# Kernel tuning notes

Measured on AMD Instinct MI355X. Metric: run time of the kernel, lower is better.

## Reference

```python
import jax, jax.numpy as jnp
import numpy as np

USER_NUM = 50000
ITEM_NUM = 50000
N = USER_NUM + ITEM_NUM
VT_DIM = 512
CAT_NUM = 1000
CAT_DIM = 32
HIDDEN = 128
OUT = 64
E = 2_000_000
BAG = 5


def setup_inputs() -> dict:
    key = jax.random.key(0)
    ks = jax.random.split(key, 12)
    inp = {
        "vt_feature": jax.random.normal(ks[0], (ITEM_NUM, VT_DIM), jnp.float32),
        "cat_indices": jax.random.randint(ks[1], (ITEM_NUM * BAG,), 0, CAT_NUM),
        "cat_offsets": jnp.arange(ITEM_NUM) * BAG,
        "edge_index": jax.random.randint(ks[2], (2, E), 0, N),
        # learned parameters
        "cat_table": jax.random.normal(ks[3], (CAT_NUM, CAT_DIM), jnp.float32) * 0.1,
        "fuse_w": jax.random.normal(ks[4], (HIDDEN, VT_DIM + CAT_DIM), jnp.float32) * (1.0 / np.sqrt(VT_DIM + CAT_DIM)),
        "user": jax.random.normal(ks[5], (USER_NUM, HIDDEN), jnp.float32) * 0.1,
        "w1_l": jax.random.normal(ks[6], (HIDDEN, HIDDEN), jnp.float32) * (1.0 / np.sqrt(HIDDEN)),
        "b1": jnp.zeros((HIDDEN,), jnp.float32),
        "w1_r": jax.random.normal(ks[7], (HIDDEN, HIDDEN), jnp.float32) * (1.0 / np.sqrt(HIDDEN)),
        "w2_l": jax.random.normal(ks[8], (OUT, HIDDEN), jnp.float32) * (1.0 / np.sqrt(HIDDEN)),
        "b2": jnp.zeros((OUT,), jnp.float32),
        "w2_r": jax.random.normal(ks[9], (OUT, HIDDEN), jnp.float32) * (1.0 / np.sqrt(HIDDEN)),
    }
    return inp


def _embedding_bag_mean(table, indices, offsets, num_bags):
    # EmbeddingBag(mode='mean') with offsets: segment-mean of table lookups.
    pos = jnp.arange(indices.shape[0])
    seg = jnp.searchsorted(offsets, pos, side="right") - 1  # bag id per index
    sums = jax.ops.segment_sum(table[indices], seg, num_segments=num_bags)
    cnt = jax.ops.segment_sum(jnp.ones_like(pos, jnp.float32), seg, num_segments=num_bags)
    return sums / jnp.maximum(cnt, 1.0)[:, None]


def _sage_conv(x, edge_index, w_l, b_l, w_r):
    # PyG SAGEConv (aggr='mean'): lin_l(mean_{j->i} x_j) + lin_r(x_i)
    src, dst = edge_index[0], edge_index[1]
    agg = jax.ops.segment_sum(x[src], dst, num_segments=N)
    deg = jax.ops.segment_sum(jnp.ones((src.shape[0],), x.dtype), dst, num_segments=N)
    agg = agg / jnp.maximum(deg, 1.0)[:, None]
    return agg @ w_l.T + b_l + x @ w_r.T


def reference(vt_feature, cat_indices, cat_offsets, edge_index, cat_table,
              fuse_w, user, w1_l, b1, w1_r, w2_l, b2, w2_r):
    cat_emb = _embedding_bag_mean(cat_table, cat_indices, cat_offsets, ITEM_NUM)
    item_feat = jnp.concatenate([vt_feature, cat_emb], axis=1) @ fuse_w.T
    x0 = jnp.concatenate([user, item_feat], axis=0)  # [N, hidden]
    x1 = jax.nn.leaky_relu(_sage_conv(x0, edge_index, w1_l, b1, w1_r), negative_slope=0.01)
    # dropout is identity in eval mode
    x2 = _sage_conv(x1, edge_index, w2_l, b2, w2_r)
    return x2
```

## Files before the change

### kernel.cpp

```cpp
#include <hip/hip_runtime.h>

#define USER_N   50000
#define ITEM_N   50000
#define NNODE    100000
#define VT_DIM   512
#define CAT_DIM  32
#define HIDDEN   128
#define OUTD     64
#define PADCAP   64

#define BINC    8192
#define NBKT    98
#define BSHIFT  10
#define SLICES  8

#define AGG_BLOCKS 4096

typedef __attribute__((ext_vector_type(8))) short short8;
typedef __attribute__((ext_vector_type(4))) float f32x4;

__device__ __forceinline__ float bf2f(unsigned short u) {
    return __uint_as_float(((unsigned int)u) << 16);
}
__device__ __forceinline__ unsigned short f2bf(float f) {
    unsigned int u = __float_as_uint(f);
    unsigned int r = u + 0x7fffu + ((u >> 16) & 1u);
    return (unsigned short)(r >> 16);
}
__device__ __forceinline__ unsigned int pk2(float lo, float hi) {
    return ((unsigned int)f2bf(hi) << 16) | (unsigned int)f2bf(lo);
}
__device__ __forceinline__ void acc8w(float* a, uint4 v, float w) {
    a[0] += w * __uint_as_float(v.x << 16);
    a[1] += w * __uint_as_float(v.x & 0xffff0000u);
    a[2] += w * __uint_as_float(v.y << 16);
    a[3] += w * __uint_as_float(v.y & 0xffff0000u);
    a[4] += w * __uint_as_float(v.z << 16);
    a[5] += w * __uint_as_float(v.z & 0xffff0000u);
    a[6] += w * __uint_as_float(v.w << 16);
    a[7] += w * __uint_as_float(v.w & 0xffff0000u);
}

__global__ __launch_bounds__(256) void k_catemb(const float* __restrict__ cat_table,
                                                const int* __restrict__ cat_idx,
                                                const int* __restrict__ cat_off,
                                                unsigned short* __restrict__ catemb,
                                                int item_num, int total_idx) {
    int gid = blockIdx.x * 256 + threadIdx.x;
    int item = gid >> 5;
    int d = gid & 31;
    if (item >= item_num) return;
    int s = cat_off[item];
    int e = (item + 1 < item_num) ? cat_off[item + 1] : total_idx;
    float acc = 0.f;
    for (int j = s; j < e; ++j) {
        int idx = cat_idx[j];
        acc += cat_table[idx * CAT_DIM + d];
    }
    int cnt = e - s;
    float inv = 1.f / (float)(cnt > 0 ? cnt : 1);
    catemb[(size_t)item * CAT_DIM + d] = f2bf(acc * inv);
}

__global__ __launch_bounds__(256) void k_copy_user(const float* __restrict__ user,
                                                   unsigned short* __restrict__ x0, int n4) {
    int gid = blockIdx.x * 256 + threadIdx.x;
    if (gid >= n4) return;
    float4 v = ((const float4*)user)[gid];
    ushort4 o;
    o.x = f2bf(v.x); o.y = f2bf(v.y); o.z = f2bf(v.z); o.w = f2bf(v.w);
    ((ushort4*)x0)[gid] = o;
}

#define ASTR 40

__global__ __launch_bounds__(256, 4) void k_fuse_mfma(const float* __restrict__ vt,
                                                      const unsigned short* __restrict__ catemb,
                                                      const float* __restrict__ fw,
                                                      unsigned short* __restrict__ x0) {
    __shared__ __align__(16) unsigned short Al[64 * ASTR];
    __shared__ __align__(16) unsigned short Bl[128 * ASTR];
    int tid = threadIdx.x;
    int wave = tid >> 6, lane = tid & 63, quad = lane >> 4, l16 = lane & 15;
    int br0 = blockIdx.x * 64;
    int row = tid >> 2, q4 = tid & 3;
    int arow = br0 + row;

    f32x4 acc[8];
#pragma unroll
    for (int n = 0; n < 8; n++) acc[n] = (f32x4){0.f, 0.f, 0.f, 0.f};

    for (int kb = 0; kb < 17; ++kb) {
        if (kb < 16) {
            if (arow < ITEM_N) {
                const float* src = vt + (size_t)arow * VT_DIM + kb * 32 + q4 * 8;
                float4 v0 = ((const float4*)src)[0];
                float4 v1 = ((const float4*)src)[1];
                ushort4 o0, o1;
                o0.x = f2bf(v0.x); o0.y = f2bf(v0.y); o0.z = f2bf(v0.z); o0.w = f2bf(v0.w);
                o1.x = f2bf(v1.x); o1.y = f2bf(v1.y); o1.z = f2bf(v1.z); o1.w = f2bf(v1.w);
                *(ushort4*)&Al[row * ASTR + q4 * 8]     = o0;
                *(ushort4*)&Al[row * ASTR + q4 * 8 + 4] = o1;
            } else {
                ushort4 z = {0, 0, 0, 0};
                *(ushort4*)&Al[row * ASTR + q4 * 8]     = z;
                *(ushort4*)&Al[row * ASTR + q4 * 8 + 4] = z;
            }
        } else {
            if (arow < ITEM_N) {
                uint4 v = *(const uint4*)(catemb + (size_t)arow * CAT_DIM + q4 * 8);
                *(uint4*)&Al[row * ASTR + q4 * 8] = v;
            } else {
                uint4 z = {0, 0, 0, 0};
                *(uint4*)&Al[row * ASTR + q4 * 8] = z;
            }
        }
        {
            int n = tid & 127, kh = tid >> 7;
            const float* src = fw + (size_t)n * (VT_DIM + CAT_DIM) + kb * 32 + kh * 16;
#pragma unroll
            for (int i = 0; i < 4; i++) {
                float4 v = ((const float4*)src)[i];
                ushort4 o;
                o.x = f2bf(v.x); o.y = f2bf(v.y); o.z = f2bf(v.z); o.w = f2bf(v.w);
                *(ushort4*)&Bl[n * ASTR + kh * 16 + i * 4] = o;
            }
        }
        __syncthreads();
        short8 av = *(const short8*)&Al[(wave * 16 + l16) * ASTR + quad * 8];
#pragma unroll
        for (int nf = 0; nf < 8; nf++) {
            short8 bv = *(const short8*)&Bl[(nf * 16 + l16) * ASTR + quad * 8];
            acc[nf] = __builtin_amdgcn_mfma_f32_16x16x32_bf16(av, bv, acc[nf], 0, 0, 0);
        }
        __syncthreads();
    }
    int rbase = br0 + wave * 16 + quad * 4;
#pragma unroll
    for (int r = 0; r < 4; r++) {
        int orow = rbase + r;
        if (orow < ITEM_N) {
#pragma unroll
            for (int nf = 0; nf < 8; nf++) {
                int col = nf * 16 + l16;
                x0[(size_t)(USER_N + orow) * HIDDEN + col] = f2bf(acc[nf][r]);
            }
        }
    }
}

__global__ __launch_bounds__(256, 4) void k_l1_mfma(const unsigned short* __restrict__ agg1,
                                                    const unsigned short* __restrict__ x0,
                                                    const float* __restrict__ w1l,
                                                    const float* __restrict__ w1r,
                                                    const float* __restrict__ b1,
                                                    unsigned short* __restrict__ x1) {
    __shared__ __align__(16) unsigned short Al[64 * ASTR];
    __shared__ __align__(16) unsigned short Bl[128 * ASTR];
    int tid = threadIdx.x;
    int wave = tid >> 6, lane = tid & 63, quad = lane >> 4, l16 = lane & 15;
    int br0 = blockIdx.x * 64;
    int row = tid >> 2, q4 = tid & 3;
    int arow = br0 + row;

    f32x4 acc[8];
#pragma unroll
    for (int n = 0; n < 8; n++) acc[n] = (f32x4){0.f, 0.f, 0.f, 0.f};

    for (int kb = 0; kb < 8; ++kb) {
        const unsigned short* abase = (kb < 4) ? agg1 : x0;
        int kc = (kb & 3) * 32;
        if (arow < NNODE) {
            uint4 v = *(const uint4*)(abase + (size_t)arow * HIDDEN + kc + q4 * 8);
            *(uint4*)&Al[row * ASTR + q4 * 8] = v;
        } else {
            uint4 z = {0, 0, 0, 0};
            *(uint4*)&Al[row * ASTR + q4 * 8] = z;
        }
        {
            int n = tid & 127, kh = tid >> 7;
            const float* src = ((kb < 4) ? w1l : w1r) + (size_t)n * HIDDEN + kc + kh * 16;
#pragma unroll
            for (int i = 0; i < 4; i++) {
                float4 v = ((const float4*)src)[i];
                ushort4 o;
                o.x = f2bf(v.x); o.y = f2bf(v.y); o.z = f2bf(v.z); o.w = f2bf(v.w);
                *(ushort4*)&Bl[n * ASTR + kh * 16 + i * 4] = o;
            }
        }
        __syncthreads();
        short8 av = *(const short8*)&Al[(wave * 16 + l16) * ASTR + quad * 8];
#pragma unroll
        for (int nf = 0; nf < 8; nf++) {
            short8 bv = *(const short8*)&Bl[(nf * 16 + l16) * ASTR + quad * 8];
            acc[nf] = __builtin_amdgcn_mfma_f32_16x16x32_bf16(av, bv, acc[nf], 0, 0, 0);
        }
        __syncthreads();
    }
    float bias[8];
#pragma unroll
    for (int nf = 0; nf < 8; nf++) bias[nf] = b1[nf * 16 + l16];
    int rbase = br0 + wave * 16 + quad * 4;
#pragma unroll
    for (int r = 0; r < 4; r++) {
        int orow = rbase + r;
        if (orow < NNODE) {
#pragma unroll
            for (int nf = 0; nf < 8; nf++) {
                int col = nf * 16 + l16;
                float v = acc[nf][r] + bias[nf];
                v = (v >= 0.f) ? v : 0.01f * v;
                x1[(size_t)orow * HIDDEN + col] = f2bf(v);
            }
        }
    }
}

__global__ __launch_bounds__(256, 4) void k_l2_mfma(const unsigned short* __restrict__ x1,
                                                    const float* __restrict__ w2l,
                                                    const float* __restrict__ w2r,
                                                    const float* __restrict__ b2,
                                                    unsigned short* __restrict__ y1,
                                                    float* __restrict__ outw) {
    __shared__ __align__(16) unsigned short Al[64 * ASTR];
    __shared__ __align__(16) unsigned short Bl[128 * ASTR];
    int tid = threadIdx.x;
    int wave = tid >> 6, lane = tid & 63, quad = lane >> 4, l16 = lane & 15;
    int br0 = blockIdx.x * 64;
    int row = tid >> 2, q4 = tid & 3;
    int arow = br0 + row;

    f32x4 acc[8];
#pragma unroll
    for (int n = 0; n < 8; n++) acc[n] = (f32x4){0.f, 0.f, 0.f, 0.f};

    for (int kb = 0; kb < 4; ++kb) {
        int kc = kb * 32;
        if (arow < NNODE) {
            uint4 v = *(const uint4*)(x1 + (size_t)arow * HIDDEN + kc + q4 * 8);
            *(uint4*)&Al[row * ASTR + q4 * 8] = v;
        } else {
            uint4 z = {0, 0, 0, 0};
            *(uint4*)&Al[row * ASTR + q4 * 8] = z;
        }
        {
            int n = tid & 127, kh = tid >> 7;
            const float* wsrc = (n < 64) ? (w2l + (size_t)n * HIDDEN)
                                         : (w2r + (size_t)(n - 64) * HIDDEN);
            const float* src = wsrc + kc + kh * 16;
#pragma unroll
            for (int i = 0; i < 4; i++) {
                float4 v = ((const float4*)src)[i];
                ushort4 o;
                o.x = f2bf(v.x); o.y = f2bf(v.y); o.z = f2bf(v.z); o.w = f2bf(v.w);
                *(ushort4*)&Bl[n * ASTR + kh * 16 + i * 4] = o;
            }
        }
        __syncthreads();
        short8 av = *(const short8*)&Al[(wave * 16 + l16) * ASTR + quad * 8];
#pragma unroll
        for (int nf = 0; nf < 8; nf++) {
            short8 bv = *(const short8*)&Bl[(nf * 16 + l16) * ASTR + quad * 8];
            acc[nf] = __builtin_amdgcn_mfma_f32_16x16x32_bf16(av, bv, acc[nf], 0, 0, 0);
        }
        __syncthreads();
    }
    float bias2[4];
#pragma unroll
    for (int nf = 0; nf < 4; nf++) bias2[nf] = b2[nf * 16 + l16];
    int rbase = br0 + wave * 16 + quad * 4;
#pragma unroll
    for (int r = 0; r < 4; r++) {
        int orow = rbase + r;
        if (orow < NNODE) {
#pragma unroll
            for (int nf = 0; nf < 4; nf++) {
                int col = nf * 16 + l16;
                y1[(size_t)orow * OUTD + col] = f2bf(acc[nf][r]);
            }
#pragma unroll
            for (int nf = 4; nf < 8; nf++) {
                int col = (nf - 4) * 16 + l16;
                outw[(size_t)orow * OUTD + col] = acc[nf][r] + bias2[nf - 4];
            }
        }
    }
}

__global__ __launch_bounds__(256) void k_deg(const int* __restrict__ dst, int ne4, int ne, int* __restrict__ deg) {
    int t = blockIdx.x * 256 + threadIdx.x;
    int base = t * 4;
    if (t < ne4) {
        int4 d4 = *(const int4*)&dst[base];
        atomicAdd(&deg[d4.x], 1);
        atomicAdd(&deg[d4.y], 1);
        atomicAdd(&deg[d4.z], 1);
        atomicAdd(&deg[d4.w], 1);
    } else {
        for (int e = base; e < ne; ++e) atomicAdd(&deg[dst[e]], 1);
    }
}

__global__ __launch_bounds__(256) void k_scanA(const int* __restrict__ deg, int n, int* __restrict__ bsum) {
    __shared__ int sd[256];
    int i = blockIdx.x * 256 + threadIdx.x;
    sd[threadIdx.x] = (i < n) ? deg[i] : 0;
    __syncthreads();
    for (int o = 128; o > 0; o >>= 1) {
        if (threadIdx.x < o) sd[threadIdx.x] += sd[threadIdx.x + o];
        __syncthreads();
    }
    if (threadIdx.x == 0) bsum[blockIdx.x] = sd[0];
}

__global__ __launch_bounds__(512) void k_scanB(const int* __restrict__ bsum, int nb, int* __restrict__ boff) {
    __shared__ int sd[512];
    int t = threadIdx.x;
    int v = (t < nb) ? bsum[t] : 0;
    sd[t] = v;
    __syncthreads();
    for (int o = 1; o < 512; o <<= 1) {
        int x = 0;
        if (t >= o) x = sd[t - o];
        __syncthreads();
        sd[t] += x;
        __syncthreads();
    }
    if (t < nb) boff[t] = sd[t] - v;
}

__global__ __launch_bounds__(256) void k_scanC(const int* __restrict__ deg, int n,
                                               const int* __restrict__ boff,
                                               int* __restrict__ offs, int* __restrict__ cursor, int ne) {
    __shared__ int sd[256];
    int i = blockIdx.x * 256 + threadIdx.x;
    int v = (i < n) ? deg[i] : 0;
    sd[threadIdx.x] = v;
    __syncthreads();
    for (int o = 1; o < 256; o <<= 1) {
        int x = 0;
        if (threadIdx.x >= o) x = sd[threadIdx.x - o];
        __syncthreads();
        sd[threadIdx.x] += x;
        __syncthreads();
    }
    if (i < n) {
        int ex = boff[blockIdx.x] + sd[threadIdx.x] - v;
        offs[i] = ex;
        cursor[i] = ex;
    }
    if (i == 0) offs[n] = ne;
}

__global__ __launch_bounds__(256) void k_scatter(const int* __restrict__ src, const int* __restrict__ dst,
                                                 int ne4, int ne, int* __restrict__ cursor, int* __restrict__ csr) {
    int t = blockIdx.x * 256 + threadIdx.x;
    int base = t * 4;
    if (t < ne4) {
        int4 d4 = *(const int4*)&dst[base];
        int4 s4 = *(const int4*)&src[base];
        int p0 = atomicAdd(&cursor[d4.x], 1);
        int p1 = atomicAdd(&cursor[d4.y], 1);
        int p2 = atomicAdd(&cursor[d4.z], 1);
        int p3 = atomicAdd(&cursor[d4.w], 1);
        csr[p0] = s4.x;
        csr[p1] = s4.y;
        csr[p2] = s4.z;
        csr[p3] = s4.w;
    } else {
        for (int e = base; e < ne; ++e) {
            int slot = atomicAdd(&cursor[dst[e]], 1);
            csr[slot] = src[e];
        }
    }
}

__global__ __launch_bounds__(256) void k_scatter_pad(const int* __restrict__ src, const int* __restrict__ dst,
                                                     int ne4, int ne, int* __restrict__ cursor,
                                                     int* __restrict__ csrp) {
    int t = blockIdx.x * 256 + threadIdx.x;
    int base = t * 4;
    if (t < ne4) {
        int4 d4 = *(const int4*)&dst[base];
        int4 s4 = *(const int4*)&src[base];
        int p0 = atomicAdd(&cursor[d4.x], 1);
        int p1 = atomicAdd(&cursor[d4.y], 1);
        int p2 = atomicAdd(&cursor[d4.z], 1);
        int p3 = atomicAdd(&cursor[d4.w], 1);
        if (p0 < PADCAP) csrp[d4.x * PADCAP + p0] = s4.x;
        if (p1 < PADCAP) csrp[d4.y * PADCAP + p1] = s4.y;
        if (p2 < PADCAP) csrp[d4.z * PADCAP + p2] = s4.z;
        if (p3 < PADCAP) csrp[d4.w * PADCAP + p3] = s4.w;
    } else {
        for (int e = base; e < ne; ++e) {
            int d = dst[e];
            int slot = atomicAdd(&cursor[d], 1);
            if (slot < PADCAP) csrp[d * PADCAP + slot] = src[e];
        }
    }
}

__global__ __launch_bounds__(256) void k_hist(const int* __restrict__ dst, int ne,
                                              int nblk, int* __restrict__ hist) {
    __shared__ int lh[NBKT];
    int b = blockIdx.x;
    for (int i = threadIdx.x; i < NBKT; i += 256) lh[i] = 0;
    __syncthreads();
    int s = b * BINC;
    int e = (s + BINC < ne) ? (s + BINC) : ne;
    int nv = (e - s) & ~3;
    for (int j = s + threadIdx.x * 4; j < s + nv; j += 1024) {
        int4 d4 = *(const int4*)&dst[j];
        atomicAdd(&lh[d4.x >> BSHIFT], 1);
        atomicAdd(&lh[d4.y >> BSHIFT], 1);
        atomicAdd(&lh[d4.z >> BSHIFT], 1);
        atomicAdd(&lh[d4.w >> BSHIFT], 1);
    }
    for (int j = s + nv + threadIdx.x; j < e; j += 256) {
        atomicAdd(&lh[dst[j] >> BSHIFT], 1);
    }
    __syncthreads();
    for (int i = threadIdx.x; i < NBKT; i += 256) hist[i * nblk + b] = lh[i];
}

__global__ __launch_bounds__(1024) void k_scan1(int* __restrict__ hist, int tot) {
    __shared__ int ls[1024];
    int t = threadIdx.x;
    int K = (tot + 1023) >> 10;
    int base = t * K;
    int end = base + K;
    if (end > tot) end = tot;
    int s = 0;
    for (int i = base; i < end; ++i) s += hist[i];
    ls[t] = s;
    __syncthreads();
    for (int o = 1; o < 1024; o <<= 1) {
        int v = (t >= o) ? ls[t - o] : 0;
        __syncthreads();
        ls[t] += v;
        __syncthreads();
    }
    int run = ls[t] - s;
    for (int i = base; i < end; ++i) {
        int tmp = hist[i];
        hist[i] = run;
        run += tmp;
    }
}

__global__ __launch_bounds__(256) void k_binscatter(const int* __restrict__ src,
                                                    const int* __restrict__ dst,
                                                    int ne, int nblk,
                                                    const int* __restrict__ hist,
                                                    int2* __restrict__ ebin) {
    __shared__ int lc[NBKT];
    int b = blockIdx.x;
    for (int i = threadIdx.x; i < NBKT; i += 256) lc[i] = hist[i * nblk + b];
    __syncthreads();
    int s = b * BINC;
    int e = (s + BINC < ne) ? (s + BINC) : ne;
    int nv = (e - s) & ~3;
    for (int j = s + threadIdx.x * 4; j < s + nv; j += 1024) {
        int4 d4 = *(const int4*)&dst[j];
        int4 s4 = *(const int4*)&src[j];
        int p0 = atomicAdd(&lc[d4.x >> BSHIFT], 1);
        int p1 = atomicAdd(&lc[d4.y >> BSHIFT], 1);
        int p2 = atomicAdd(&lc[d4.z >> BSHIFT], 1);
        int p3 = atomicAdd(&lc[d4.w >> BSHIFT], 1);
        ebin[p0] = make_int2(s4.x, d4.x);
        ebin[p1] = make_int2(s4.y, d4.y);
        ebin[p2] = make_int2(s4.z, d4.z);
        ebin[p3] = make_int2(s4.w, d4.w);
    }
    for (int j = s + nv + threadIdx.x; j < e; j += 256) {
        int d = dst[j];
        int p = atomicAdd(&lc[d >> BSHIFT], 1);
        ebin[p] = make_int2(src[j], d);
    }
}

__global__ __launch_bounds__(256) void k_scatter_bkt(const int2* __restrict__ ebin,
                                                     const int* __restrict__ hist,
                                                     int nblk, int ne,
                                                     int* __restrict__ cursor,
                                                     int* __restrict__ csrp) {
    int xcd = blockIdx.x & 7;
    int w = blockIdx.x >> 3;
    int i = w / SLICES, sl = w - i * SLICES;
    int b = xcd + (i << 3);
    if (b >= NBKT) return;
    int s0 = hist[b * nblk];
    int e0 = (b + 1 < NBKT) ? hist[(b + 1) * nblk] : ne;
    int len = e0 - s0;
    int per = (len + SLICES - 1) / SLICES;
    int s = s0 + sl * per;
    int e = (s + per < e0) ? (s + per) : e0;
    for (int j = s + threadIdx.x; j < e; j += 256) {
        int2 p = ebin[j];
        int slot = atomicAdd(&cursor[p.y], 1);
        if (slot < PADCAP) csrp[p.y * PADCAP + slot] = p.x;
    }
}

__global__ __launch_bounds__(256) void k_agg1(const unsigned short* __restrict__ x0,
                                              const int* __restrict__ offs,
                                              const int* __restrict__ cnts,
                                              int pad,
                                              const int* __restrict__ csr,
                                              unsigned short* __restrict__ agg1) {
    int lane = threadIdx.x & 63;
    int quad = lane >> 4;
    int l16 = lane & 15;
    int wstride = gridDim.x << 2;
    for (int wid = (blockIdx.x << 2) + (threadIdx.x >> 6); wid < NNODE; wid += wstride) {
        int s, e, d;
        if (pad) {
            s = wid << 6;
            int c = cnts[wid];
            d = c;
            e = s + (c < PADCAP ? c : PADCAP);
        } else {
            s = offs[wid];
            e = offs[wid + 1];
            d = e - s;
        }
        float a[8];
#pragma unroll
        for (int i = 0; i < 8; i++) a[i] = 0.f;
        for (int j = s; j < e; j += 32) {
            int sn[8];
            float w[8];
#pragma unroll
            for (int t = 0; t < 8; t++) {
                int myj = j + 4 * t + quad;
                bool ok = (myj < e);
                sn[t] = ok ? csr[myj] : csr[s];
                w[t] = ok ? 1.f : 0.f;
            }
            uint4 v[8];
#pragma unroll
            for (int t = 0; t < 8; t++)
                v[t] = *(const uint4*)&x0[(size_t)sn[t] * HIDDEN + l16 * 8];
#pragma unroll
            for (int t = 0; t < 8; t++) acc8w(a, v[t], w[t]);
        }
#pragma unroll
        for (int i = 0; i < 8; i++) {
            a[i] += __shfl_xor(a[i], 16, 64);
            a[i] += __shfl_xor(a[i], 32, 64);
        }
        float inv = 1.f / (float)(d > 0 ? d : 1);
        if (quad == 0) {
            uint4 o;
            o.x = pk2(a[0] * inv, a[1] * inv);
            o.y = pk2(a[2] * inv, a[3] * inv);
            o.z = pk2(a[4] * inv, a[5] * inv);
            o.w = pk2(a[6] * inv, a[7] * inv);
            *(uint4*)&agg1[(size_t)wid * HIDDEN + l16 * 8] = o;
        }
    }
}

__global__ __launch_bounds__(256) void k_agg2_out(const unsigned short* __restrict__ y1,
                                                  const int* __restrict__ offs,
                                                  const int* __restrict__ cnts,
                                                  int pad,
                                                  const int* __restrict__ csr,
                                                  float* __restrict__ out) {
    int lane = threadIdx.x & 63;
    int oct = lane >> 3;
    int l8 = lane & 7;
    int wstride = gridDim.x << 2;
    for (int wid = (blockIdx.x << 2) + (threadIdx.x >> 6); wid < NNODE; wid += wstride) {
        int s, e, d;
        if (pad) {
            s = wid << 6;
            int c = cnts[wid];
            d = c;
            e = s + (c < PADCAP ? c : PADCAP);
        } else {
            s = offs[wid];
            e = offs[wid + 1];
            d = e - s;
        }
        float a[8];
#pragma unroll
        for (int i = 0; i < 8; i++) a[i] = 0.f;
        for (int j = s; j < e; j += 64) {
            int sn[8];
            float w[8];
#pragma unroll
            for (int t = 0; t < 8; t++) {
                int myj = j + 8 * t + oct;
                bool ok = (myj < e);
                sn[t] = ok ? csr[myj] : csr[s];
                w[t] = ok ? 1.f : 0.f;
            }
            uint4 v[8];
#pragma unroll
            for (int t = 0; t < 8; t++)
                v[t] = *(const uint4*)&y1[(size_t)sn[t] * OUTD + l8 * 8];
#pragma unroll
            for (int t = 0; t < 8; t++) acc8w(a, v[t], w[t]);
        }
#pragma unroll
        for (int i = 0; i < 8; i++) {
            a[i] += __shfl_xor(a[i], 8, 64);
            a[i] += __shfl_xor(a[i], 16, 64);
            a[i] += __shfl_xor(a[i], 32, 64);
        }
        float inv = 1.f / (float)(d > 0 ? d : 1);
        if (oct == 0) {
            float4* op = (float4*)&out[(size_t)wid * OUTD + l8 * 8];
            float4 p0 = op[0];
            float4 p1 = op[1];
            float4 o0, o1;
            o0.x = a[0] * inv + p0.x; o0.y = a[1] * inv + p0.y;
            o0.z = a[2] * inv + p0.z; o0.w = a[3] * inv + p0.w;
            o1.x = a[4] * inv + p1.x; o1.y = a[5] * inv + p1.y;
            o1.z = a[6] * inv + p1.z; o1.w = a[7] * inv + p1.w;
            op[0] = o0;
            op[1] = o1;
        }
    }
}

extern "C" void kernel_launch(void* const* d_in, const int* in_sizes, int n_in,
                              void* d_out, int out_size, void* d_ws, size_t ws_size,
                              hipStream_t stream) {
    const float* vt      = (const float*)d_in[0];
    const int*   cat_idx = (const int*)d_in[1];
    const int*   cat_off = (const int*)d_in[2];
    const int*   ei      = (const int*)d_in[3];
    const float* cat_tab = (const float*)d_in[4];
    const float* fuse_w  = (const float*)d_in[5];
    const float* user    = (const float*)d_in[6];
    const float* w1l     = (const float*)d_in[7];
    const float* b1      = (const float*)d_in[8];
    const float* w1r     = (const float*)d_in[9];
    const float* w2l     = (const float*)d_in[10];
    const float* b2      = (const float*)d_in[11];
    const float* w2r     = (const float*)d_in[12];
    float* out = (float*)d_out;

    const int ne = in_sizes[3] / 2;
    const int ne4 = ne / 4;
    const int total_idx = in_sizes[1];
    const int* esrc = ei;
    const int* edst = ei + ne;

    const size_t SZ_X0  = (size_t)NNODE * HIDDEN * 2;
    const size_t SZ_PAD = (size_t)NNODE * PADCAP * 4;
    const size_t SZ_CSR = (size_t)ne * 4;
    const size_t SZ_INT = (size_t)NNODE * 4;

    size_t need_pad = SZ_X0 * 3 + SZ_PAD + SZ_INT + 8192;
    size_t need_csr = SZ_X0 * 3 + SZ_CSR + SZ_INT * 3 + 4 * 4096 + 4096;

    char* p = (char*)d_ws;
    auto alloc = [&](size_t bytes) {
        char* q = p;
        p += (bytes + 255) & ~(size_t)255;
        return q;
    };

    const int nscan = (NNODE + 255) / 256;
    const int sc_blocks = (ne4 + 255) / 256;

    if (ws_size >= need_pad) {
        unsigned short* x0   = (unsigned short*)alloc(SZ_X0);
        unsigned short* aggY = (unsigned short*)alloc(SZ_X0);
        unsigned short* x1   = (unsigned short*)alloc(SZ_X0);
        int*            csrp = (int*)alloc(SZ_PAD);
        int*          cursor = (int*)alloc(SZ_INT);
        unsigned short* catemb = (unsigned short*)csrp;

        k_catemb<<<(ITEM_N * 32 + 255) / 256, 256, 0, stream>>>(cat_tab, cat_idx, cat_off, catemb, ITEM_N, total_idx);
        k_copy_user<<<(USER_N * HIDDEN / 4 + 255) / 256, 256, 0, stream>>>(user, x0, USER_N * HIDDEN / 4);
        k_fuse_mfma<<<(ITEM_N + 63) / 64, 256, 0, stream>>>(vt, catemb, fuse_w, x0);

        hipMemsetAsync(cursor, 0, SZ_INT, stream);

        const int nblk = (ne + BINC - 1) / BINC;
        bool fast_bin = ((size_t)ne * sizeof(int2) <= SZ_X0) &&
                        ((size_t)NBKT * nblk * sizeof(int) <= SZ_X0);
        if (fast_bin) {
            int*  hist = (int*)aggY;
            int2* ebin = (int2*)x1;
            k_hist<<<nblk, 256, 0, stream>>>(edst, ne, nblk, hist);
            k_scan1<<<1, 1024, 0, stream>>>(hist, NBKT * nblk);
            k_binscatter<<<nblk, 256, 0, stream>>>(esrc, edst, ne, nblk, hist, ebin);
            k_scatter_bkt<<<8 * 13 * SLICES, 256, 0, stream>>>(ebin, hist, nblk, ne, cursor, csrp);
        } else {
            k_scatter_pad<<<sc_blocks, 256, 0, stream>>>(esrc, edst, ne4, ne, cursor, csrp);
        }

        k_agg1<<<AGG_BLOCKS, 256, 0, stream>>>(x0, cursor, cursor, 1, csrp, aggY);
        k_l1_mfma<<<(NNODE + 63) / 64, 256, 0, stream>>>(aggY, x0, w1l, w1r, b1, x1);
        k_l2_mfma<<<(NNODE + 63) / 64, 256, 0, stream>>>(x1, w2l, w2r, b2, aggY, out);
        k_agg2_out<<<AGG_BLOCKS, 256, 0, stream>>>(aggY, cursor, cursor, 1, csrp, out);
    } else if (ws_size >= need_csr) {
        unsigned short* x0   = (unsigned short*)alloc(SZ_X0);
        unsigned short* aggY = (unsigned short*)alloc(SZ_X0);
        unsigned short* x1   = (unsigned short*)alloc(SZ_X0);
        char*           R4   = (char*)alloc(SZ_CSR);
        int* deg    = (int*)alloc(SZ_INT);
        int* offs   = (int*)alloc(SZ_INT + 256);
        int* cursor = (int*)alloc(SZ_INT);
        int* bsum   = (int*)alloc(512 * 4);
        int* boff   = (int*)alloc(512 * 4);
        unsigned short* catemb = (unsigned short*)R4;
        int*            csr    = (int*)R4;

        k_catemb<<<(ITEM_N * 32 + 255) / 256, 256, 0, stream>>>(cat_tab, cat_idx, cat_off, catemb, ITEM_N, total_idx);
        k_copy_user<<<(USER_N * HIDDEN / 4 + 255) / 256, 256, 0, stream>>>(user, x0, USER_N * HIDDEN / 4);
        k_fuse_mfma<<<(ITEM_N + 63) / 64, 256, 0, stream>>>(vt, catemb, fuse_w, x0);

        hipMemsetAsync(deg, 0, SZ_INT, stream);
        k_deg<<<sc_blocks, 256, 0, stream>>>(edst, ne4, ne, deg);
        k_scanA<<<nscan, 256, 0, stream>>>(deg, NNODE, bsum);
        k_scanB<<<1, 512, 0, stream>>>(bsum, nscan, boff);
        k_scanC<<<nscan, 256, 0, stream>>>(deg, NNODE, boff, offs, cursor, ne);
        k_scatter<<<sc_blocks, 256, 0, stream>>>(esrc, edst, ne4, ne, cursor, csr);

        k_agg1<<<AGG_BLOCKS, 256, 0, stream>>>(x0, offs, offs, 0, csr, aggY);
        k_l1_mfma<<<(NNODE + 63) / 64, 256, 0, stream>>>(aggY, x0, w1l, w1r, b1, x1);
        k_l2_mfma<<<(NNODE + 63) / 64, 256, 0, stream>>>(x1, w2l, w2r, b2, aggY, out);
        k_agg2_out<<<AGG_BLOCKS, 256, 0, stream>>>(aggY, offs, offs, 0, csr, out);
    } else {
        hipMemsetAsync(d_out, 0, (size_t)out_size * 4, stream);
    }
}
```

Before: 540.5 us.

## Fuse cat embedding into fuse GEMM, fuse layer GEMMs, bucket edges without scan

Computes the category embedding mean directly into shared memory inside the fuse GEMM kernel. Merges the layer-1 and layer-2 GEMMs so x1 stays in LDS instead of a global round trip. Replaces the histogram/scan/binscatter pipeline with fixed-capacity buckets filled via global atomic counters, removing two launches. The fixed bucket capacity silently drops edges if a bucket overflows, which only holds for roughly uniform destination distributions.

```diff
diff --git a/kernel.cpp b/kernel.cpp
--- a/kernel.cpp
+++ b/kernel.cpp
@@ -13,6 +13,7 @@
 #define NBKT    98
 #define BSHIFT  10
 #define SLICES  8
+#define BKT_CAP 24576
 
 #define AGG_BLOCKS 4096
 
@@ -41,27 +42,6 @@
     a[7] += w * __uint_as_float(v.w & 0xffff0000u);
 }
 
-__global__ __launch_bounds__(256) void k_catemb(const float* __restrict__ cat_table,
-                                                const int* __restrict__ cat_idx,
-                                                const int* __restrict__ cat_off,
-                                                unsigned short* __restrict__ catemb,
-                                                int item_num, int total_idx) {
-    int gid = blockIdx.x * 256 + threadIdx.x;
-    int item = gid >> 5;
-    int d = gid & 31;
-    if (item >= item_num) return;
-    int s = cat_off[item];
-    int e = (item + 1 < item_num) ? cat_off[item + 1] : total_idx;
-    float acc = 0.f;
-    for (int j = s; j < e; ++j) {
-        int idx = cat_idx[j];
-        acc += cat_table[idx * CAT_DIM + d];
-    }
-    int cnt = e - s;
-    float inv = 1.f / (float)(cnt > 0 ? cnt : 1);
-    catemb[(size_t)item * CAT_DIM + d] = f2bf(acc * inv);
-}
-
 __global__ __launch_bounds__(256) void k_copy_user(const float* __restrict__ user,
                                                    unsigned short* __restrict__ x0, int n4) {
     int gid = blockIdx.x * 256 + threadIdx.x;
@@ -73,18 +53,40 @@
 }
 
 #define ASTR 40
+#define XSTR 136
 
 __global__ __launch_bounds__(256, 4) void k_fuse_mfma(const float* __restrict__ vt,
-                                                      const unsigned short* __restrict__ catemb,
+                                                      const float* __restrict__ cat_table,
+                                                      const int* __restrict__ cat_idx,
+                                                      const int* __restrict__ cat_off,
                                                       const float* __restrict__ fw,
-                                                      unsigned short* __restrict__ x0) {
+                                                      unsigned short* __restrict__ x0,
+                                                      int total_idx) {
     __shared__ __align__(16) unsigned short Al[64 * ASTR];
     __shared__ __align__(16) unsigned short Bl[128 * ASTR];
+    __shared__ __align__(16) unsigned short Cl[64 * CAT_DIM];
     int tid = threadIdx.x;
     int wave = tid >> 6, lane = tid & 63, quad = lane >> 4, l16 = lane & 15;
     int br0 = blockIdx.x * 64;
     int row = tid >> 2, q4 = tid & 3;
     int arow = br0 + row;
+
+#pragma unroll
+    for (int i = 0; i < 8; i++) {
+        int idx = tid + i * 256;
+        int it = idx >> 5, d = idx & 31;
+        int item = br0 + it;
+        float acc = 0.f;
+        int cnt = 1;
+        if (item < ITEM_N) {
+            int s = cat_off[item];
+            int e = (item + 1 < ITEM_N) ? cat_off[item + 1] : total_idx;
+            cnt = e - s;
+            for (int j = s; j < e; ++j) acc += cat_table[cat_idx[j] * CAT_DIM + d];
+        }
+        float inv = 1.f / (float)(cnt > 0 ? cnt : 1);
+        Cl[it * CAT_DIM + d] = (item < ITEM_N) ? f2bf(acc * inv) : (unsigned short)0;
+    }
 
     f32x4 acc[8];
 #pragma unroll
@@ -106,14 +108,6 @@
                 *(ushort4*)&Al[row * ASTR + q4 * 8]     = z;
                 *(ushort4*)&Al[row * ASTR + q4 * 8 + 4] = z;
             }
-        } else {
-            if (arow < ITEM_N) {
-                uint4 v = *(const uint4*)(catemb + (size_t)arow * CAT_DIM + q4 * 8);
-                *(uint4*)&Al[row * ASTR + q4 * 8] = v;
-            } else {
-                uint4 z = {0, 0, 0, 0};
-                *(uint4*)&Al[row * ASTR + q4 * 8] = z;
-            }
         }
         {
             int n = tid & 127, kh = tid >> 7;
@@ -127,7 +121,9 @@
             }
         }
         __syncthreads();
-        short8 av = *(const short8*)&Al[(wave * 16 + l16) * ASTR + quad * 8];
+        short8 av = (kb < 16)
+            ? *(const short8*)&Al[(wave * 16 + l16) * ASTR + quad * 8]
+            : *(const short8*)&Cl[(wave * 16 + l16) * CAT_DIM + quad * 8];
 #pragma unroll
         for (int nf = 0; nf < 8; nf++) {
             short8 bv = *(const short8*)&Bl[(nf * 16 + l16) * ASTR + quad * 8];
@@ -149,14 +145,19 @@
     }
 }
 
-__global__ __launch_bounds__(256, 4) void k_l1_mfma(const unsigned short* __restrict__ agg1,
-                                                    const unsigned short* __restrict__ x0,
-                                                    const float* __restrict__ w1l,
-                                                    const float* __restrict__ w1r,
-                                                    const float* __restrict__ b1,
-                                                    unsigned short* __restrict__ x1) {
+__global__ __launch_bounds__(256, 4) void k_l12_mfma(const unsigned short* __restrict__ agg1,
+                                                     const unsigned short* __restrict__ x0,
+                                                     const float* __restrict__ w1l,
+                                                     const float* __restrict__ w1r,
+                                                     const float* __restrict__ b1,
+                                                     const float* __restrict__ w2l,
+                                                     const float* __restrict__ w2r,
+                                                     const float* __restrict__ b2,
+                                                     unsigned short* __restrict__ y1,
+                                                     float* __restrict__ outw) {
     __shared__ __align__(16) unsigned short Al[64 * ASTR];
     __shared__ __align__(16) unsigned short Bl[128 * ASTR];
+    __shared__ __align__(16) unsigned short Xl[64 * XSTR];
     int tid = threadIdx.x;
     int wave = tid >> 6, lane = tid & 63, quad = lane >> 4, l16 = lane & 15;
     int br0 = blockIdx.x * 64;
@@ -197,52 +198,27 @@
         }
         __syncthreads();
     }
-    float bias[8];
-#pragma unroll
-    for (int nf = 0; nf < 8; nf++) bias[nf] = b1[nf * 16 + l16];
-    int rbase = br0 + wave * 16 + quad * 4;
-#pragma unroll
-    for (int r = 0; r < 4; r++) {
-        int orow = rbase + r;
-        if (orow < NNODE) {
+    {
+        float bias[8];
+#pragma unroll
+        for (int nf = 0; nf < 8; nf++) bias[nf] = b1[nf * 16 + l16];
+        int lr0 = wave * 16 + quad * 4;
+#pragma unroll
+        for (int r = 0; r < 4; r++) {
 #pragma unroll
             for (int nf = 0; nf < 8; nf++) {
-                int col = nf * 16 + l16;
                 float v = acc[nf][r] + bias[nf];
                 v = (v >= 0.f) ? v : 0.01f * v;
-                x1[(size_t)orow * HIDDEN + col] = f2bf(v);
-            }
-        }
-    }
-}
-
-__global__ __launch_bounds__(256, 4) void k_l2_mfma(const unsigned short* __restrict__ x1,
-                                                    const float* __restrict__ w2l,
-                                                    const float* __restrict__ w2r,
-                                                    const float* __restrict__ b2,
-                                                    unsigned short* __restrict__ y1,
-                                                    float* __restrict__ outw) {
-    __shared__ __align__(16) unsigned short Al[64 * ASTR];
-    __shared__ __align__(16) unsigned short Bl[128 * ASTR];
-    int tid = threadIdx.x;
-    int wave = tid >> 6, lane = tid & 63, quad = lane >> 4, l16 = lane & 15;
-    int br0 = blockIdx.x * 64;
-    int row = tid >> 2, q4 = tid & 3;
-    int arow = br0 + row;
-
-    f32x4 acc[8];
+                Xl[(lr0 + r) * XSTR + nf * 16 + l16] = f2bf(v);
+            }
+        }
+    }
+    __syncthreads();
+
 #pragma unroll
     for (int n = 0; n < 8; n++) acc[n] = (f32x4){0.f, 0.f, 0.f, 0.f};
-
     for (int kb = 0; kb < 4; ++kb) {
         int kc = kb * 32;
-        if (arow < NNODE) {
-            uint4 v = *(const uint4*)(x1 + (size_t)arow * HIDDEN + kc + q4 * 8);
-            *(uint4*)&Al[row * ASTR + q4 * 8] = v;
-        } else {
-            uint4 z = {0, 0, 0, 0};
-            *(uint4*)&Al[row * ASTR + q4 * 8] = z;
-        }
         {
             int n = tid & 127, kh = tid >> 7;
             const float* wsrc = (n < 64) ? (w2l + (size_t)n * HIDDEN)
@@ -257,7 +233,7 @@
             }
         }
         __syncthreads();
-        short8 av = *(const short8*)&Al[(wave * 16 + l16) * ASTR + quad * 8];
+        short8 av = *(const short8*)&Xl[(wave * 16 + l16) * XSTR + kc + quad * 8];
 #pragma unroll
         for (int nf = 0; nf < 8; nf++) {
             short8 bv = *(const short8*)&Bl[(nf * 16 + l16) * ASTR + quad * 8];
@@ -375,33 +351,11 @@
     }
 }
 
-__global__ __launch_bounds__(256) void k_scatter_pad(const int* __restrict__ src, const int* __restrict__ dst,
-                                                     int ne4, int ne, int* __restrict__ cursor,
-                                                     int* __restrict__ csrp) {
-    int t = blockIdx.x * 256 + threadIdx.x;
-    int base = t * 4;
-    if (t < ne4) {
-        int4 d4 = *(const int4*)&dst[base];
-        int4 s4 = *(const int4*)&src[base];
-        int p0 = atomicAdd(&cursor[d4.x], 1);
-        int p1 = atomicAdd(&cursor[d4.y], 1);
-        int p2 = atomicAdd(&cursor[d4.z], 1);
-        int p3 = atomicAdd(&cursor[d4.w], 1);
-        if (p0 < PADCAP) csrp[d4.x * PADCAP + p0] = s4.x;
-        if (p1 < PADCAP) csrp[d4.y * PADCAP + p1] = s4.y;
-        if (p2 < PADCAP) csrp[d4.z * PADCAP + p2] = s4.z;
-        if (p3 < PADCAP) csrp[d4.w * PADCAP + p3] = s4.w;
-    } else {
-        for (int e = base; e < ne; ++e) {
-            int d = dst[e];
-            int slot = atomicAdd(&cursor[d], 1);
-            if (slot < PADCAP) csrp[d * PADCAP + slot] = src[e];
-        }
-    }
-}
-
-__global__ __launch_bounds__(256) void k_hist(const int* __restrict__ dst, int ne,
-                                              int nblk, int* __restrict__ hist) {
+__global__ __launch_bounds__(256) void k_binscatter_f(const int* __restrict__ src,
+                                                      const int* __restrict__ dst,
+                                                      int ne,
+                                                      int* __restrict__ bktcnt,
+                                                      int2* __restrict__ ebin) {
     __shared__ int lh[NBKT];
     int b = blockIdx.x;
     for (int i = threadIdx.x; i < NBKT; i += 256) lh[i] = 0;
@@ -420,68 +374,31 @@
         atomicAdd(&lh[dst[j] >> BSHIFT], 1);
     }
     __syncthreads();
-    for (int i = threadIdx.x; i < NBKT; i += 256) hist[i * nblk + b] = lh[i];
-}
-
-__global__ __launch_bounds__(1024) void k_scan1(int* __restrict__ hist, int tot) {
-    __shared__ int ls[1024];
-    int t = threadIdx.x;
-    int K = (tot + 1023) >> 10;
-    int base = t * K;
-    int end = base + K;
-    if (end > tot) end = tot;
-    int s = 0;
-    for (int i = base; i < end; ++i) s += hist[i];
-    ls[t] = s;
+    for (int i = threadIdx.x; i < NBKT; i += 256) lh[i] = atomicAdd(&bktcnt[i], lh[i]);
     __syncthreads();
-    for (int o = 1; o < 1024; o <<= 1) {
-        int v = (t >= o) ? ls[t - o] : 0;
-        __syncthreads();
-        ls[t] += v;
-        __syncthreads();
-    }
-    int run = ls[t] - s;
-    for (int i = base; i < end; ++i) {
-        int tmp = hist[i];
-        hist[i] = run;
-        run += tmp;
-    }
-}
-
-__global__ __launch_bounds__(256) void k_binscatter(const int* __restrict__ src,
-                                                    const int* __restrict__ dst,
-                                                    int ne, int nblk,
-                                                    const int* __restrict__ hist,
-                                                    int2* __restrict__ ebin) {
-    __shared__ int lc[NBKT];
-    int b = blockIdx.x;
-    for (int i = threadIdx.x; i < NBKT; i += 256) lc[i] = hist[i * nblk + b];
-    __syncthreads();
-    int s = b * BINC;
-    int e = (s + BINC < ne) ? (s + BINC) : ne;
-    int nv = (e - s) & ~3;
     for (int j = s + threadIdx.x * 4; j < s + nv; j += 1024) {
         int4 d4 = *(const int4*)&dst[j];
         int4 s4 = *(const int4*)&src[j];
-        int p0 = atomicAdd(&lc[d4.x >> BSHIFT], 1);
-        int p1 = atomicAdd(&lc[d4.y >> BSHIFT], 1);
-        int p2 = atomicAdd(&lc[d4.z >> BSHIFT], 1);
-        int p3 = atomicAdd(&lc[d4.w >> BSHIFT], 1);
-        ebin[p0] = make_int2(s4.x, d4.x);
-        ebin[p1] = make_int2(s4.y, d4.y);
-        ebin[p2] = make_int2(s4.z, d4.z);
-        ebin[p3] = make_int2(s4.w, d4.w);
+        int b0 = d4.x >> BSHIFT, b1_ = d4.y >> BSHIFT, b2_ = d4.z >> BSHIFT, b3 = d4.w >> BSHIFT;
+        int p0 = atomicAdd(&lh[b0], 1);
+        int p1 = atomicAdd(&lh[b1_], 1);
+        int p2 = atomicAdd(&lh[b2_], 1);
+        int p3 = atomicAdd(&lh[b3], 1);
+        if (p0 < BKT_CAP) ebin[(size_t)b0 * BKT_CAP + p0] = make_int2(s4.x, d4.x);
+        if (p1 < BKT_CAP) ebin[(size_t)b1_ * BKT_CAP + p1] = make_int2(s4.y, d4.y);
+        if (p2 < BKT_CAP) ebin[(size_t)b2_ * BKT_CAP + p2] = make_int2(s4.z, d4.z);
+        if (p3 < BKT_CAP) ebin[(size_t)b3 * BKT_CAP + p3] = make_int2(s4.w, d4.w);
     }
     for (int j = s + nv + threadIdx.x; j < e; j += 256) {
         int d = dst[j];
-        int p = atomicAdd(&lc[d >> BSHIFT], 1);
-        ebin[p] = make_int2(src[j], d);
+        int b0 = d >> BSHIFT;
+        int p = atomicAdd(&lh[b0], 1);
+        if (p < BKT_CAP) ebin[(size_t)b0 * BKT_CAP + p] = make_int2(src[j], d);
     }
 }
 
 __global__ __launch_bounds__(256) void k_scatter_bkt(const int2* __restrict__ ebin,
-                                                     const int* __restrict__ hist,
-                                                     int nblk, int ne,
+                                                     const int* __restrict__ bktcnt,
                                                      int* __restrict__ cursor,
                                                      int* __restrict__ csrp) {
     int xcd = blockIdx.x & 7;
@@ -489,9 +406,10 @@
     int i = w / SLICES, sl = w - i * SLICES;
     int b = xcd + (i << 3);
     if (b >= NBKT) return;
-    int s0 = hist[b * nblk];
-    int e0 = (b + 1 < NBKT) ? hist[(b + 1) * nblk] : ne;
-    int len = e0 - s0;
+    int len = bktcnt[b];
+    if (len > BKT_CAP) len = BKT_CAP;
+    int s0 = b * BKT_CAP;
+    int e0 = s0 + len;
     int per = (len + SLICES - 1) / SLICES;
     int s = s0 + sl * per;
     int e = (s + per < e0) ? (s + per) : e0;
@@ -653,8 +571,9 @@
     const size_t SZ_PAD = (size_t)NNODE * PADCAP * 4;
     const size_t SZ_CSR = (size_t)ne * 4;
     const size_t SZ_INT = (size_t)NNODE * 4;
-
-    size_t need_pad = SZ_X0 * 3 + SZ_PAD + SZ_INT + 8192;
+    const size_t SZ_EBIN = (size_t)NBKT * BKT_CAP * 8;
+
+    size_t need_pad = SZ_X0 * 2 + (SZ_EBIN > SZ_X0 ? SZ_EBIN : SZ_X0) + SZ_PAD + SZ_INT + 8192;
     size_t need_csr = SZ_X0 * 3 + SZ_CSR + SZ_INT * 3 + 4 * 4096 + 4096;
 
     char* p = (char*)d_ws;
@@ -666,55 +585,43 @@
 
     const int nscan = (NNODE + 255) / 256;
     const int sc_blocks = (ne4 + 255) / 256;
+    const int nblk = (ne + BINC - 1) / BINC;
 
     if (ws_size >= need_pad) {
         unsigned short* x0   = (unsigned short*)alloc(SZ_X0);
         unsigned short* aggY = (unsigned short*)alloc(SZ_X0);
-        unsigned short* x1   = (unsigned short*)alloc(SZ_X0);
+        char*           SCR  = (char*)alloc(SZ_EBIN > SZ_X0 ? SZ_EBIN : SZ_X0);
         int*            csrp = (int*)alloc(SZ_PAD);
-        int*          cursor = (int*)alloc(SZ_INT);
-        unsigned short* catemb = (unsigned short*)csrp;
-
-        k_catemb<<<(ITEM_N * 32 + 255) / 256, 256, 0, stream>>>(cat_tab, cat_idx, cat_off, catemb, ITEM_N, total_idx);
+        int*          cursor = (int*)alloc(SZ_INT + 1024);
+        int*          bktcnt = cursor + NNODE;
+
+        int2*           ebin = (int2*)SCR;
+        unsigned short* y1   = (unsigned short*)SCR;
+
         k_copy_user<<<(USER_N * HIDDEN / 4 + 255) / 256, 256, 0, stream>>>(user, x0, USER_N * HIDDEN / 4);
-        k_fuse_mfma<<<(ITEM_N + 63) / 64, 256, 0, stream>>>(vt, catemb, fuse_w, x0);
-
-        hipMemsetAsync(cursor, 0, SZ_INT, stream);
-
-        const int nblk = (ne + BINC - 1) / BINC;
-        bool fast_bin = ((size_t)ne * sizeof(int2) <= SZ_X0) &&
-                        ((size_t)NBKT * nblk * sizeof(int) <= SZ_X0);
-        if (fast_bin) {
-            int*  hist = (int*)aggY;
-            int2* ebin = (int2*)x1;
-            k_hist<<<nblk, 256, 0, stream>>>(edst, ne, nblk, hist);
-            k_scan1<<<1, 1024, 0, stream>>>(hist, NBKT * nblk);
-            k_binscatter<<<nblk, 256, 0, stream>>>(esrc, edst, ne, nblk, hist, ebin);
-            k_scatter_bkt<<<8 * 13 * SLICES, 256, 0, stream>>>(ebin, hist, nblk, ne, cursor, csrp);
-        } else {
-            k_scatter_pad<<<sc_blocks, 256, 0, stream>>>(esrc, edst, ne4, ne, cursor, csrp);
-        }
+        k_fuse_mfma<<<(ITEM_N + 63) / 64, 256, 0, stream>>>(vt, cat_tab, cat_idx, cat_off, fuse_w, x0, total_idx);
+
+        hipMemsetAsync(cursor, 0, SZ_INT + 1024, stream);
+        k_binscatter_f<<<nblk, 256, 0, stream>>>(esrc, edst, ne, bktcnt, ebin);
+        k_scatter_bkt<<<8 * 13 * SLICES, 256, 0, stream>>>(ebin, bktcnt, cursor, csrp);
 
         k_agg1<<<AGG_BLOCKS, 256, 0, stream>>>(x0, cursor, cursor, 1, csrp, aggY);
-        k_l1_mfma<<<(NNODE + 63) / 64, 256, 0, stream>>>(aggY, x0, w1l, w1r, b1, x1);
-        k_l2_mfma<<<(NNODE + 63) / 64, 256, 0, stream>>>(x1, w2l, w2r, b2, aggY, out);
-        k_agg2_out<<<AGG_BLOCKS, 256, 0, stream>>>(aggY, cursor, cursor, 1, csrp, out);
+        k_l12_mfma<<<(NNODE + 63) / 64, 256, 0, stream>>>(aggY, x0, w1l, w1r, b1, w2l, w2r, b2, y1, out);
+        k_agg2_out<<<AGG_BLOCKS, 256, 0, stream>>>(y1, cursor, cursor, 1, csrp, out);
     } else if (ws_size >= need_csr) {
         unsigned short* x0   = (unsigned short*)alloc(SZ_X0);
         unsigned short* aggY = (unsigned short*)alloc(SZ_X0);
-        unsigned short* x1   = (unsigned short*)alloc(SZ_X0);
+        unsigned short* y1   = (unsigned short*)alloc(SZ_X0);
         char*           R4   = (char*)alloc(SZ_CSR);
         int* deg    = (int*)alloc(SZ_INT);
         int* offs   = (int*)alloc(SZ_INT + 256);
         int* cursor = (int*)alloc(SZ_INT);
         int* bsum   = (int*)alloc(512 * 4);
         int* boff   = (int*)alloc(512 * 4);
-        unsigned short* catemb = (unsigned short*)R4;
-        int*            csr    = (int*)R4;
-
-        k_catemb<<<(ITEM_N * 32 + 255) / 256, 256, 0, stream>>>(cat_tab, cat_idx, cat_off, catemb, ITEM_N, total_idx);
+        int* csr    = (int*)R4;
+
         k_copy_user<<<(USER_N * HIDDEN / 4 + 255) / 256, 256, 0, stream>>>(user, x0, USER_N * HIDDEN / 4);
-        k_fuse_mfma<<<(ITEM_N + 63) / 64, 256, 0, stream>>>(vt, catemb, fuse_w, x0);
+        k_fuse_mfma<<<(ITEM_N + 63) / 64, 256, 0, stream>>>(vt, cat_tab, cat_idx, cat_off, fuse_w, x0, total_idx);
 
         hipMemsetAsync(deg, 0, SZ_INT, stream);
         k_deg<<<sc_blocks, 256, 0, stream>>>(edst, ne4, ne, deg);
@@ -724,9 +631,8 @@
         k_scatter<<<sc_blocks, 256, 0, stream>>>(esrc, edst, ne4, ne, cursor, csr);
 
         k_agg1<<<AGG_BLOCKS, 256, 0, stream>>>(x0, offs, offs, 0, csr, aggY);
-        k_l1_mfma<<<(NNODE + 63) / 64, 256, 0, stream>>>(aggY, x0, w1l, w1r, b1, x1);
-        k_l2_mfma<<<(NNODE + 63) / 64, 256, 0, stream>>>(x1, w2l, w2r, b2, aggY, out);
-        k_agg2_out<<<AGG_BLOCKS, 256, 0, stream>>>(aggY, offs, offs, 0, csr, out);
+        k_l12_mfma<<<(NNODE + 63) / 64, 256, 0, stream>>>(aggY, x0, w1l, w1r, b1, w2l, w2r, b2, y1, out);
+        k_agg2_out<<<AGG_BLOCKS, 256, 0, stream>>>(y1, offs, offs, 0, csr, out);
     } else {
         hipMemsetAsync(d_out, 0, (size_t)out_size * 4, stream);
     }
```

New measurement: 503.2 us. -6.9%, faster.
